# Performance work log

Measured on AMD Instinct MI355X. Metric: run time of the kernel, lower is better.

The kernel has to match this reference:

```python
import jax, jax.numpy as jnp
import numpy as np

D_MODEL = 1024
N_HEADS = 16
DFF = 4096
B, S = 2, 2048
EPS = 1e-6


def _dense_params(key, d_in, d_out):
    kw, kb = jax.random.split(key)
    w = jax.random.normal(kw, (d_in, d_out), jnp.float32) * 0.02
    b = jax.random.normal(kb, (d_out,), jnp.float32) * 0.02
    return w, b


def setup_inputs() -> dict:
    key = jax.random.key(0)
    ks = jax.random.split(key, 20)
    inp = {
        "x": jax.random.normal(ks[0], (B, S, D_MODEL), jnp.float32),
        "enc_output": jax.random.normal(ks[1], (B, S, D_MODEL), jnp.float32),
        # causal look-ahead mask: 1 where attention is NOT allowed
        "look_ahead_mask": jnp.triu(jnp.ones((S, S), jnp.float32), k=1)[None, None],
        "padding_mask": (jax.random.uniform(ks[2], (B, 1, 1, S)) < 0.1).astype(jnp.float32),
    }
    names = ["mha1_wq", "mha1_wk", "mha1_wv", "mha1_wo",
             "mha2_wq", "mha2_wk", "mha2_wv", "mha2_wo"]
    for i, n in enumerate(names):
        w, b = _dense_params(ks[3 + i], D_MODEL, D_MODEL)
        inp[n] = w
        inp[n.replace("w", "b")] = b
    inp["ffn_w1"], inp["ffn_b1"] = _dense_params(ks[11], D_MODEL, DFF)
    inp["ffn_w2"], inp["ffn_b2"] = _dense_params(ks[12], DFF, D_MODEL)
    for i, n in enumerate(["ln1", "ln2", "ln3"]):
        inp[n + "_g"] = jnp.ones((D_MODEL,), jnp.float32)
        inp[n + "_b"] = jnp.zeros((D_MODEL,), jnp.float32)
    return inp


def _layernorm(x, g, b):
    mu = jnp.mean(x, axis=-1, keepdims=True)
    var = jnp.mean(jnp.square(x - mu), axis=-1, keepdims=True)
    return (x - mu) * jax.lax.rsqrt(var + EPS) * g + b


def _mha(v, k, q, mask, wq, bq, wk, bk, wv, bv, wo, bo):
    Bq, Sq, D = q.shape
    depth = D // N_HEADS

    def split(t):  # [B,S,D] -> [B,H,S,depth]
        return t.reshape(t.shape[0], -1, N_HEADS, depth).transpose(0, 2, 1, 3)

    qh = split(q @ wq + bq)
    kh = split(k @ wk + bk)
    vh = split(v @ wv + bv)
    logits = jnp.einsum("bhqd,bhkd->bhqk", qh, kh) / jnp.sqrt(jnp.float32(depth))
    if mask is not None:
        logits = logits + mask * (-1e9)
    attn = jax.nn.softmax(logits, axis=-1)
    out = jnp.einsum("bhqk,bhkd->bhqd", attn, vh)
    out = out.transpose(0, 2, 1, 3).reshape(Bq, Sq, D)
    return out @ wo + bo


def reference(x, enc_output, look_ahead_mask, padding_mask,
              mha1_wq, mha1_bq, mha1_wk, mha1_bk, mha1_wv, mha1_bv, mha1_wo, mha1_bo,
              mha2_wq, mha2_bq, mha2_wk, mha2_bk, mha2_wv, mha2_bv, mha2_wo, mha2_bo,
              ffn_w1, ffn_b1, ffn_w2, ffn_b2,
              ln1_g, ln1_b, ln2_g, ln2_b, ln3_g, ln3_b):
    # self-attention (training=False -> dropout is identity)
    attn1 = _mha(x, x, x, look_ahead_mask,
                 mha1_wq, mha1_bq, mha1_wk, mha1_bk, mha1_wv, mha1_bv, mha1_wo, mha1_bo)
    out1 = _layernorm(x + attn1, ln1_g, ln1_b)
    # cross-attention: q from decoder, k/v from encoder output
    attn2 = _mha(enc_output, enc_output, out1, padding_mask,
                 mha2_wq, mha2_bq, mha2_wk, mha2_bk, mha2_wv, mha2_bv, mha2_wo, mha2_bo)
    out2 = _layernorm(out1 + attn2, ln2_g, ln2_b)
    ffn = jax.nn.relu(out2 @ ffn_w1 + ffn_b1) @ ffn_w2 + ffn_b2
    return _layernorm(out2 + ffn, ln3_g, ln3_b)
```

## Files before the change

### kernel.cpp

```cpp
#include <hip/hip_runtime.h>
#include <hip/hip_bf16.h>
#include <stdint.h>

#define DM   1024
#define NH   16
#define SS   2048
#define BB   2
#define MT   4096

typedef __attribute__((ext_vector_type(8))) short short8;
typedef __attribute__((ext_vector_type(4))) float f32x4;

typedef __attribute__((address_space(1))) const unsigned int as1_uint;
typedef __attribute__((address_space(3))) unsigned int as3_uint;

__device__ __forceinline__ void async16(const void* g, void* l) {
  __builtin_amdgcn_global_load_lds((as1_uint*)g, (as3_uint*)l, 16, 0, 0);
}

__device__ __forceinline__ unsigned short f2bf(float f) {
  union { float f; unsigned u; } c; c.f = f;
  unsigned r = c.u + 0x7fffu + ((c.u >> 16) & 1u);
  return (unsigned short)(r >> 16);
}

__device__ __forceinline__ unsigned cvt_pk_bf16(float lo, float hi) {
  unsigned r;
  asm("v_cvt_pk_bf16_f32 %0, %1, %2" : "=v"(r) : "v"(lo), "v"(hi));
  return r;
}

__global__ __launch_bounds__(256) void k_f32_to_bf16(
    const float* __restrict__ in, unsigned short* __restrict__ out, int n) {
  int i = (blockIdx.x * 256 + threadIdx.x) * 4;
  if (i >= n) return;
  float4 v = *(const float4*)(in + i);
  uint2 u;
  u.x = (unsigned)f2bf(v.x) | ((unsigned)f2bf(v.y) << 16);
  u.y = (unsigned)f2bf(v.z) | ((unsigned)f2bf(v.w) << 16);
  *(uint2*)(out + i) = u;
}

__global__ __launch_bounds__(256) void k_transpose_bf16(
    const float* __restrict__ in, unsigned short* __restrict__ out, int R, int C) {
  __shared__ float t[32][33];
  int c0 = blockIdx.x * 32, r0 = blockIdx.y * 32;
  int tx = threadIdx.x, ty = threadIdx.y;
#pragma unroll
  for (int i = 0; i < 4; i++)
    t[ty + i * 8][tx] = in[(size_t)(r0 + ty + i * 8) * C + c0 + tx];
  __syncthreads();
#pragma unroll
  for (int i = 0; i < 4; i++)
    out[(size_t)(c0 + ty + i * 8) * R + r0 + tx] = f2bf(t[tx][ty + i * 8]);
}

template<int BM, int OUT_MODE, bool RELU, bool RESID, bool SPLITK>
__global__ __launch_bounds__(256) void k_gemm(
    const unsigned short* __restrict__ A,
    const unsigned short* __restrict__ Bt,
    const float* __restrict__ bias,
    const float* __restrict__ resid,
    void* __restrict__ outp, void* __restrict__ outp2,
    int M, int N, int K, int KS) {
  __shared__ unsigned short Alds[2][BM * 32];
  __shared__ unsigned short Blds[2][128 * 32];
  int tid = threadIdx.x;
  int w = tid >> 6, lane = tid & 63;
  int l15 = lane & 15, l4 = lane >> 4;
  int brow = blockIdx.y * BM, bcol = blockIdx.x * 128;

  constexpr int MR = 4;
  constexpr int NR = (BM == 128) ? 4 : 2;
  int wr = (BM == 128) ? (w >> 1) : 0;
  int wc = (BM == 128) ? (w & 1) : w;
  int rbase = wr * 64;
  int cbase = wc * (NR * 16);

  f32x4 acc[MR][NR];
#pragma unroll
  for (int i = 0; i < MR; i++)
#pragma unroll
    for (int j = 0; j < NR; j++) acc[i][j] = (f32x4){0.f, 0.f, 0.f, 0.f};

#define STAGEG(bufi, kk) do {                                                  \
    _Pragma("unroll")                                                          \
    for (int c = 0; c < BM / 64; c++) {                                        \
      int elem = (c * 256 + tid) * 8;                                          \
      int row = elem >> 5, col = elem & 31;                                    \
      async16(A + (size_t)(brow + row) * K + (kk) + col, &Alds[bufi][elem]);   \
    }                                                                          \
    _Pragma("unroll")                                                          \
    for (int c = 0; c < 2; c++) {                                              \
      int elem = (c * 256 + tid) * 8;                                          \
      int row = elem >> 5, col = elem & 31;                                    \
      async16(Bt + (size_t)(bcol + row) * K + (kk) + col, &Blds[bufi][elem]);  \
    } } while (0)

  int kbeg = SPLITK ? blockIdx.z * KS : 0;
  int kend = kbeg + KS;
  STAGEG(0, kbeg);
  __syncthreads();
  int cur = 0;
  for (int k0 = kbeg; k0 < kend; k0 += 32) {
    if (k0 + 32 < kend) STAGEG(cur ^ 1, k0 + 32);
    short8 af[MR], bfr[NR];
#pragma unroll
    for (int i = 0; i < MR; i++)
      af[i] = *(const short8*)&Alds[cur][(rbase + i * 16 + l15) * 32 + l4 * 8];
#pragma unroll
    for (int j = 0; j < NR; j++)
      bfr[j] = *(const short8*)&Blds[cur][(cbase + j * 16 + l15) * 32 + l4 * 8];
#pragma unroll
    for (int i = 0; i < MR; i++)
#pragma unroll
      for (int j = 0; j < NR; j++)
        acc[i][j] = __builtin_amdgcn_mfma_f32_16x16x32_bf16(af[i], bfr[j], acc[i][j], 0, 0, 0);
    __syncthreads();
    cur ^= 1;
  }
#undef STAGEG

  void* op = (SPLITK && blockIdx.z) ? outp2 : outp;
#pragma unroll
  for (int i = 0; i < MR; i++)
#pragma unroll
    for (int j = 0; j < NR; j++) {
      int row = brow + rbase + i * 16 + l4 * 4;
      int col = bcol + cbase + j * 16 + l15;
      float bs = (SPLITK || !bias) ? 0.f : bias[col];
#pragma unroll
      for (int r = 0; r < 4; r++) {
        float v = acc[i][j][r] + bs;
        if (RESID) v += resid[(size_t)(row + r) * N + col];
        if (RELU) v = fmaxf(v, 0.f);
        if (OUT_MODE == 0) ((float*)op)[(size_t)(row + r) * N + col] = v;
        else               ((unsigned short*)op)[(size_t)(row + r) * N + col] = f2bf(v);
      }
    }
}

template<int NMAT>
__global__ __launch_bounds__(256) void k_gemm_qkv(
    const unsigned short* __restrict__ A,
    const unsigned short* __restrict__ Bt,
    const float* __restrict__ b0, const float* __restrict__ b1, const float* __restrict__ b2,
    unsigned short* __restrict__ o0, unsigned short* __restrict__ o1, unsigned short* __restrict__ o2,
    int vmat, int M, int K) {
  __shared__ unsigned short Alds[2][128 * 32];
  __shared__ unsigned short Blds[2][128 * 32];
  int tid = threadIdx.x;
  int w = tid >> 6, lane = tid & 63;
  int wr = w >> 1, wc = w & 1;
  int l15 = lane & 15, l4 = lane >> 4;
  int brow = blockIdx.y * 128, bcol = blockIdx.x * 128;

  f32x4 acc[4][4];
#pragma unroll
  for (int i = 0; i < 4; i++)
#pragma unroll
    for (int j = 0; j < 4; j++) acc[i][j] = (f32x4){0.f, 0.f, 0.f, 0.f};

#define STAGEQ(bufi, kk) do {                                                  \
    _Pragma("unroll")                                                          \
    for (int c = 0; c < 2; c++) {                                              \
      int elem = (c * 256 + tid) * 8;                                          \
      int row = elem >> 5, col = elem & 31;                                    \
      async16(A + (size_t)(brow + row) * K + (kk) + col, &Alds[bufi][elem]);   \
      async16(Bt + (size_t)(bcol + row) * K + (kk) + col, &Blds[bufi][elem]);  \
    } } while (0)

  STAGEQ(0, 0);
  __syncthreads();
  int cur = 0;
  for (int k0 = 0; k0 < K; k0 += 32) {
    if (k0 + 32 < K) STAGEQ(cur ^ 1, k0 + 32);
    short8 af[4], bfr[4];
#pragma unroll
    for (int i = 0; i < 4; i++) {
      af[i]  = *(const short8*)&Alds[cur][(wr * 64 + i * 16 + l15) * 32 + l4 * 8];
      bfr[i] = *(const short8*)&Blds[cur][(wc * 64 + i * 16 + l15) * 32 + l4 * 8];
    }
#pragma unroll
    for (int i = 0; i < 4; i++)
#pragma unroll
      for (int j = 0; j < 4; j++)
        acc[i][j] = __builtin_amdgcn_mfma_f32_16x16x32_bf16(af[i], bfr[j], acc[i][j], 0, 0, 0);
    __syncthreads();
    cur ^= 1;
  }
#undef STAGEQ

  int mat = bcol >> 10;
  const float* bias = (mat == 0) ? b0 : (mat == 1) ? b1 : b2;
  unsigned short* op = (mat == 0) ? o0 : (mat == 1) ? o1 : o2;
  int colSlab = bcol & 1023;
  bool tr = (mat == vmat);
#pragma unroll
  for (int i = 0; i < 4; i++)
#pragma unroll
    for (int j = 0; j < 4; j++) {
      int row = brow + wr * 64 + i * 16 + l4 * 4;
      int colL = colSlab + wc * 64 + j * 16 + l15;
      float bs = bias[colL];
#pragma unroll
      for (int r = 0; r < 4; r++) {
        float v = acc[i][j][r] + bs;
        if (tr) op[(size_t)colL * M + row + r] = f2bf(v);
        else    op[(size_t)(row + r) * 1024 + colL] = f2bf(v);
      }
    }
}

template<bool CAUSAL>
__global__ __launch_bounds__(256) void k_attn(
    const unsigned short* __restrict__ Q,
    const unsigned short* __restrict__ Kb,
    const unsigned short* __restrict__ Vt,
    const float* __restrict__ pm,
    unsigned short* __restrict__ out) {
  __shared__ unsigned short Klds[2][64 * 64];
  __shared__ unsigned short Vlds[2][64 * 64];
  __shared__ unsigned short Pw[4][2][16 * 72];
  int tid = threadIdx.x, w = tid >> 6, lane = tid & 63;
  int l15 = lane & 15, l4 = lane >> 4;
  int qt = CAUSAL ? ((int)gridDim.x - 1 - (int)blockIdx.x) : blockIdx.x;
  int h = blockIdx.y, b = blockIdx.z;
  int qbase = qt * 128 + w * 32;
  const float SC = 0.125f * 1.44269504089f;

  short8 qf[2][2];
#pragma unroll
  for (int f = 0; f < 2; f++) {
    size_t qrow = (size_t)b * SS + qbase + f * 16 + l15;
#pragma unroll
    for (int ks = 0; ks < 2; ks++)
      qf[f][ks] = *(const short8*)(Q + qrow * DM + h * 64 + ks * 32 + l4 * 8);
  }

  float mrow[2] = {-1e30f, -1e30f}, lrow[2] = {0.f, 0.f};
  f32x4 accO[2][4];
#pragma unroll
  for (int f = 0; f < 2; f++)
#pragma unroll
    for (int d = 0; d < 4; d++) accO[f][d] = (f32x4){0.f, 0.f, 0.f, 0.f};

#define STAGE(bufi, kt_) do {                                                  \
    _Pragma("unroll")                                                          \
    for (int c = 0; c < 2; c++) {                                              \
      int e0 = w * 1024 + c * 512;                                             \
      int elem = e0 + lane * 8;                                                \
      int row_ = elem >> 6;                                                    \
      int col_ = (elem & 63) ^ ((row_ & 7) << 3);                              \
      async16(Kb + (size_t)(b * SS + (kt_) * 64 + row_) * DM + h * 64 + col_,  \
              &Klds[bufi][elem]);                                              \
      async16(Vt + (size_t)(h * 64 + row_) * MT + b * SS + (kt_) * 64 + col_,  \
              &Vlds[bufi][elem]);                                              \
    } } while (0)

  int ktend = CAUSAL ? (2 * qt + 1) : (SS / 64 - 1);
  STAGE(0, 0);
  __syncthreads();
  int cur = 0;

  for (int kt = 0; kt <= ktend; kt++) {
    if (kt < ktend) STAGE(cur ^ 1, kt + 1);

    bool active = !CAUSAL || (kt * 64 <= qbase + 31);
    if (active) {
      f32x4 sa[2][4];
#pragma unroll
      for (int f = 0; f < 2; f++)
#pragma unroll
        for (int nt = 0; nt < 4; nt++) sa[f][nt] = (f32x4){0.f, 0.f, 0.f, 0.f};
      __builtin_amdgcn_s_setprio(1);
#pragma unroll
      for (int ks = 0; ks < 2; ks++)
#pragma unroll
        for (int nt = 0; nt < 4; nt++) {
          int kr = nt * 16 + l15;
          short8 kf = *(const short8*)&Klds[cur][kr * 64 + ((ks * 32 + l4 * 8) ^ ((kr & 7) << 3))];
#pragma unroll
          for (int f = 0; f < 2; f++)
            sa[f][nt] = __builtin_amdgcn_mfma_f32_16x16x32_bf16(kf, qf[f][ks], sa[f][nt], 0, 0, 0);
        }
      __builtin_amdgcn_s_setprio(0);

      float pmb[16];
      if (!CAUSAL) {
#pragma unroll
        for (int nt = 0; nt < 4; nt++) {
          float4 pmv = *(const float4*)(pm + b * SS + kt * 64 + nt * 16 + l4 * 4);
#pragma unroll
          for (int r = 0; r < 4; r++) pmb[nt * 4 + r] = ((const float*)&pmv)[r] * -1e30f;
        }
      }
      bool diag = CAUSAL && (kt * 64 + 63 > qbase);

#pragma unroll
      for (int f = 0; f < 2; f++) {
        float sv[16], tmax = -3e38f;
        if (CAUSAL && !diag) {
#pragma unroll
          for (int i = 0; i < 16; i++) {
            float s = sa[f][i >> 2][i & 3] * SC;
            sv[i] = s; tmax = fmaxf(tmax, s);
          }
        } else if (CAUSAL) {
#pragma unroll
          for (int nt = 0; nt < 4; nt++)
#pragma unroll
            for (int r = 0; r < 4; r++) {
              float s = sa[f][nt][r] * SC;
              int kg = kt * 64 + nt * 16 + l4 * 4 + r;
              int qg = qbase + f * 16 + l15;
              if (kg > qg) s = -1e30f;
              sv[nt * 4 + r] = s; tmax = fmaxf(tmax, s);
            }
        } else {
#pragma unroll
          for (int i = 0; i < 16; i++) {
            float s = fmaf(sa[f][i >> 2][i & 3], SC, pmb[i]);
            sv[i] = s; tmax = fmaxf(tmax, s);
          }
        }
        tmax = fmaxf(tmax, __shfl_xor(tmax, 16));
        tmax = fmaxf(tmax, __shfl_xor(tmax, 32));

        if (!__all(tmax - mrow[f] <= 8.f)) {
          float mnew = fmaxf(mrow[f], tmax);
          float corr = exp2f(mrow[f] - mnew);
          mrow[f] = mnew;
          lrow[f] *= corr;
#pragma unroll
          for (int r = 0; r < 4; r++) {
            float cq = __shfl(corr, l4 * 4 + r);
#pragma unroll
            for (int dt = 0; dt < 4; dt++) accO[f][dt][r] *= cq;
          }
        }

        float p[16], psum = 0.f;
#pragma unroll
        for (int i = 0; i < 16; i++) { p[i] = exp2f(sv[i] - mrow[f]); psum += p[i]; }
        psum += __shfl_xor(psum, 16);
        psum += __shfl_xor(psum, 32);
        lrow[f] += psum;

#pragma unroll
        for (int nt = 0; nt < 4; nt++) {
          uint2 u;
          u.x = cvt_pk_bf16(p[nt * 4 + 0], p[nt * 4 + 1]);
          u.y = cvt_pk_bf16(p[nt * 4 + 2], p[nt * 4 + 3]);
          *(uint2*)&Pw[w][f][l15 * 72 + nt * 16 + l4 * 4] = u;
        }
      }

      __builtin_amdgcn_s_setprio(1);
#pragma unroll
      for (int ks = 0; ks < 2; ks++) {
        short8 pf0 = *(const short8*)&Pw[w][0][l15 * 72 + ks * 32 + l4 * 8];
        short8 pf1 = *(const short8*)&Pw[w][1][l15 * 72 + ks * 32 + l4 * 8];
#pragma unroll
        for (int dt = 0; dt < 4; dt++) {
          int vr = dt * 16 + l15;
          short8 vf = *(const short8*)&Vlds[cur][vr * 64 + ((ks * 32 + l4 * 8) ^ ((vr & 7) << 3))];
          accO[0][dt] = __builtin_amdgcn_mfma_f32_16x16x32_bf16(pf0, vf, accO[0][dt], 0, 0, 0);
          accO[1][dt] = __builtin_amdgcn_mfma_f32_16x16x32_bf16(pf1, vf, accO[1][dt], 0, 0, 0);
        }
      }
      __builtin_amdgcn_s_setprio(0);
    }
    __syncthreads();
    cur ^= 1;
  }
#undef STAGE

#pragma unroll
  for (int f = 0; f < 2; f++)
#pragma unroll
    for (int r = 0; r < 4; r++) {
      float lq = __shfl(lrow[f], l4 * 4 + r);
      float inv = 1.f / lq;
      size_t row = (size_t)b * SS + qbase + f * 16 + l4 * 4 + r;
#pragma unroll
      for (int dt = 0; dt < 4; dt++)
        out[row * DM + h * 64 + dt * 16 + l15] = f2bf(accO[f][dt][r] * inv);
    }
}

__global__ __launch_bounds__(256) void k_ln(
    const float* __restrict__ in, const float* __restrict__ in2,
    const float* __restrict__ resid, const float* __restrict__ bias,
    const float* __restrict__ g, const float* __restrict__ bb,
    float* __restrict__ outf, unsigned short* __restrict__ outb) {
  int row = blockIdx.x, tid = threadIdx.x;
  int w = tid >> 6;
  __shared__ float red[4];
  float4 v = *(const float4*)(in + (size_t)row * 1024 + tid * 4);
  if (in2) {
    float4 v2 = *(const float4*)(in2 + (size_t)row * 1024 + tid * 4);
    v.x += v2.x; v.y += v2.y; v.z += v2.z; v.w += v2.w;
  }
  if (resid) {
    float4 v2 = *(const float4*)(resid + (size_t)row * 1024 + tid * 4);
    v.x += v2.x; v.y += v2.y; v.z += v2.z; v.w += v2.w;
  }
  if (bias) {
    float4 v2 = *(const float4*)(bias + tid * 4);
    v.x += v2.x; v.y += v2.y; v.z += v2.z; v.w += v2.w;
  }
  float s = v.x + v.y + v.z + v.w;
#pragma unroll
  for (int d = 1; d < 64; d <<= 1) s += __shfl_xor(s, d);
  if ((tid & 63) == 0) red[w] = s;
  __syncthreads();
  float mu = (red[0] + red[1] + red[2] + red[3]) * (1.f / 1024.f);
  float d0 = v.x - mu, d1 = v.y - mu, d2 = v.z - mu, d3 = v.w - mu;
  float q = d0 * d0 + d1 * d1 + d2 * d2 + d3 * d3;
#pragma unroll
  for (int d = 1; d < 64; d <<= 1) q += __shfl_xor(q, d);
  __syncthreads();
  if ((tid & 63) == 0) red[w] = q;
  __syncthreads();
  float var = (red[0] + red[1] + red[2] + red[3]) * (1.f / 1024.f);
  float rs = rsqrtf(var + 1e-6f);
  float4 gg = *(const float4*)(g + tid * 4);
  float4 bv = *(const float4*)(bb + tid * 4);
  float y0 = d0 * rs * gg.x + bv.x;
  float y1 = d1 * rs * gg.y + bv.y;
  float y2 = d2 * rs * gg.z + bv.z;
  float y3 = d3 * rs * gg.w + bv.w;
  if (outf) {
    float4 o; o.x = y0; o.y = y1; o.z = y2; o.w = y3;
    *(float4*)(outf + (size_t)row * 1024 + tid * 4) = o;
  }
  if (outb) {
    uint2 u;
    u.x = (unsigned)f2bf(y0) | ((unsigned)f2bf(y1) << 16);
    u.y = (unsigned)f2bf(y2) | ((unsigned)f2bf(y3) << 16);
    *(uint2*)(outb + (size_t)row * 1024 + tid * 4) = u;
  }
}

extern "C" void kernel_launch(void* const* d_in, const int* in_sizes, int n_in,
                              void* d_out, int out_size, void* d_ws, size_t ws_size,
                              hipStream_t stream) {
  const float* x    = (const float*)d_in[0];
  const float* enc  = (const float*)d_in[1];
  const float* pm   = (const float*)d_in[3];
  const float* wq1  = (const float*)d_in[4];   const float* bq1 = (const float*)d_in[5];
  const float* wk1  = (const float*)d_in[6];   const float* bk1 = (const float*)d_in[7];
  const float* wv1  = (const float*)d_in[8];   const float* bv1 = (const float*)d_in[9];
  const float* wo1  = (const float*)d_in[10];  const float* bo1 = (const float*)d_in[11];
  const float* wq2  = (const float*)d_in[12];  const float* bq2 = (const float*)d_in[13];
  const float* wk2  = (const float*)d_in[14];  const float* bk2 = (const float*)d_in[15];
  const float* wv2  = (const float*)d_in[16];  const float* bv2 = (const float*)d_in[17];
  const float* wo2  = (const float*)d_in[18];  const float* bo2 = (const float*)d_in[19];
  const float* fw1  = (const float*)d_in[20];  const float* fb1 = (const float*)d_in[21];
  const float* fw2  = (const float*)d_in[22];  const float* fb2 = (const float*)d_in[23];
  const float* ln1g = (const float*)d_in[24];  const float* ln1b = (const float*)d_in[25];
  const float* ln2g = (const float*)d_in[26];  const float* ln2b = (const float*)d_in[27];
  const float* ln3g = (const float*)d_in[28];  const float* ln3b = (const float*)d_in[29];

  char* ws = (char*)d_ws;
  unsigned short* XB = (unsigned short*)(ws + 0);
  unsigned short* EB = (unsigned short*)(ws + 8388608);
  unsigned short* Qb = (unsigned short*)(ws + 16777216);
  unsigned short* Kb = (unsigned short*)(ws + 25165824);
  unsigned short* Vt = (unsigned short*)(ws + 33554432);
  unsigned short* AT = (unsigned short*)(ws + 41943040);
  float*          T  = (float*)(ws + 50331648);
  float*          R  = (float*)(ws + 67108864);
  unsigned short* RB = (unsigned short*)(ws + 83886080);
  unsigned short* WT0 = (unsigned short*)(ws + 92274688);
  unsigned short* W1T = (unsigned short*)(ws + 92274688 + 16777216);
  unsigned short* W2T = (unsigned short*)(ws + 92274688 + 25165824);
  unsigned short* H   = (unsigned short*)(ws + 0);
  float*          T1  = (float*)(ws + 33554432);

  k_f32_to_bf16<<<4096, 256, 0, stream>>>(x, XB, MT * DM);
  k_f32_to_bf16<<<4096, 256, 0, stream>>>(enc, EB, MT * DM);
  dim3 tb(32, 8);
  const float* wlist[8] = {wq1, wk1, wv1, wo1, wq2, wk2, wv2, wo2};
  for (int i = 0; i < 8; i++)
    k_transpose_bf16<<<dim3(32, 32), tb, 0, stream>>>(wlist[i], WT0 + (size_t)i * 1048576, 1024, 1024);
  k_transpose_bf16<<<dim3(128, 32), tb, 0, stream>>>(fw1, W1T, 1024, 4096);
  k_transpose_bf16<<<dim3(32, 128), tb, 0, stream>>>(fw2, W2T, 4096, 1024);

  dim3 g64(8, 64), ga(16, 16, 2);

  k_gemm_qkv<3><<<dim3(24, 32), 256, 0, stream>>>(XB, WT0, bq1, bk1, bv1,
                                                  Qb, Kb, Vt, 2, MT, DM);
  k_attn<true><<<ga, 256, 0, stream>>>(Qb, Kb, Vt, nullptr, AT);
  k_gemm<64, 0, false, true, false><<<g64, 256, 0, stream>>>(
      AT, WT0 + 3 * 1048576, bo1, x, T, nullptr, MT, DM, DM, DM);
  k_ln<<<4096, 256, 0, stream>>>(T, nullptr, nullptr, nullptr, ln1g, ln1b, R, RB);

  k_gemm<64, 1, false, false, false><<<g64, 256, 0, stream>>>(
      RB, WT0 + 4 * 1048576, bq2, nullptr, Qb, nullptr, MT, DM, DM, DM);
  k_gemm_qkv<2><<<dim3(16, 32), 256, 0, stream>>>(EB, WT0 + 5 * 1048576, bk2, bv2, nullptr,
                                                  Kb, Vt, nullptr, 1, MT, DM);
  k_attn<false><<<ga, 256, 0, stream>>>(Qb, Kb, Vt, pm, AT);
  k_gemm<64, 0, false, true, false><<<g64, 256, 0, stream>>>(
      AT, WT0 + 7 * 1048576, bo2, R, T, nullptr, MT, DM, DM, DM);
  k_ln<<<4096, 256, 0, stream>>>(T, nullptr, nullptr, nullptr, ln2g, ln2b, R, RB);

  k_gemm<128, 1, true, false, false><<<dim3(32, 32), 256, 0, stream>>>(
      RB, W1T, fb1, nullptr, H, nullptr, MT, 4096, DM, DM);
  k_gemm<128, 0, false, false, true><<<dim3(8, 32, 2), 256, 0, stream>>>(
      H, W2T, nullptr, nullptr, T, T1, MT, DM, 4096, 2048);
  k_ln<<<4096, 256, 0, stream>>>(T, T1, R, fb2, ln3g, ln3b, (float*)d_out, nullptr);
}
```

Baseline: 507.0 us.

## Triple-buffer GEMM and attention loads, batch QKV via grid z, split-K out-projections

Replaces double buffering with a three-stage LDS ring in the GEMM, QKV GEMM and attention kernels. Each loop waits on vmcnt and issues a raw s_barrier instead of a full __syncthreads, so loads stay in flight two iterations ahead. The QKV kernel now picks its matrix from blockIdx.z, which lets the cross-attention Q, K and V projections run in one launch. The output projections become split-K GEMMs whose bias and residual are folded into the layernorm, and FFN2 uses the 64-row tile. The cost is more LDS per block, which may lower occupancy, and the hand-placed waitcnt depends on exact load counts being right.

```diff
diff --git a/kernel.cpp b/kernel.cpp
--- a/kernel.cpp
+++ b/kernel.cpp
@@ -17,6 +17,9 @@
 __device__ __forceinline__ void async16(const void* g, void* l) {
   __builtin_amdgcn_global_load_lds((as1_uint*)g, (as3_uint*)l, 16, 0, 0);
 }
+
+#define WAITV(n) asm volatile("s_waitcnt vmcnt(" #n ")" ::: "memory")
+#define BARRIER_SB() do { __builtin_amdgcn_s_barrier(); __builtin_amdgcn_sched_barrier(0); } while (0)
 
 __device__ __forceinline__ unsigned short f2bf(float f) {
   union { float f; unsigned u; } c; c.f = f;
@@ -63,8 +66,8 @@
     const float* __restrict__ resid,
     void* __restrict__ outp, void* __restrict__ outp2,
     int M, int N, int K, int KS) {
-  __shared__ unsigned short Alds[2][BM * 32];
-  __shared__ unsigned short Blds[2][128 * 32];
+  __shared__ unsigned short Alds[3][BM * 32];
+  __shared__ unsigned short Blds[3][128 * 32];
   int tid = threadIdx.x;
   int w = tid >> 6, lane = tid & 63;
   int l15 = lane & 15, l4 = lane >> 4;
@@ -98,26 +101,37 @@
     } } while (0)
 
   int kbeg = SPLITK ? blockIdx.z * KS : 0;
-  int kend = kbeg + KS;
+  int nk = KS / 32;
   STAGEG(0, kbeg);
-  __syncthreads();
-  int cur = 0;
-  for (int k0 = kbeg; k0 < kend; k0 += 32) {
-    if (k0 + 32 < kend) STAGEG(cur ^ 1, k0 + 32);
+  if (nk > 1) {
+    STAGEG(1, kbeg + 32);
+    if (BM == 128) WAITV(4); else WAITV(3);
+  } else {
+    WAITV(0);
+  }
+  BARRIER_SB();
+
+  for (int t = 0; t < nk; t++) {
+    int buf = t % 3;
+    if (t + 2 < nk) STAGEG((t + 2) % 3, kbeg + (t + 2) * 32);
     short8 af[MR], bfr[NR];
 #pragma unroll
     for (int i = 0; i < MR; i++)
-      af[i] = *(const short8*)&Alds[cur][(rbase + i * 16 + l15) * 32 + l4 * 8];
+      af[i] = *(const short8*)&Alds[buf][(rbase + i * 16 + l15) * 32 + l4 * 8];
 #pragma unroll
     for (int j = 0; j < NR; j++)
-      bfr[j] = *(const short8*)&Blds[cur][(cbase + j * 16 + l15) * 32 + l4 * 8];
+      bfr[j] = *(const short8*)&Blds[buf][(cbase + j * 16 + l15) * 32 + l4 * 8];
 #pragma unroll
     for (int i = 0; i < MR; i++)
 #pragma unroll
       for (int j = 0; j < NR; j++)
         acc[i][j] = __builtin_amdgcn_mfma_f32_16x16x32_bf16(af[i], bfr[j], acc[i][j], 0, 0, 0);
-    __syncthreads();
-    cur ^= 1;
+    if (t + 2 < nk) {
+      if (BM == 128) WAITV(4); else WAITV(3);
+    } else if (t + 1 < nk) {
+      WAITV(0);
+    }
+    if (t + 1 < nk) BARRIER_SB();
   }
 #undef STAGEG
 
@@ -140,19 +154,22 @@
     }
 }
 
-template<int NMAT>
 __global__ __launch_bounds__(256) void k_gemm_qkv(
-    const unsigned short* __restrict__ A,
+    const unsigned short* __restrict__ a0, const unsigned short* __restrict__ a1,
+    const unsigned short* __restrict__ a2,
     const unsigned short* __restrict__ Bt,
     const float* __restrict__ b0, const float* __restrict__ b1, const float* __restrict__ b2,
     unsigned short* __restrict__ o0, unsigned short* __restrict__ o1, unsigned short* __restrict__ o2,
     int vmat, int M, int K) {
-  __shared__ unsigned short Alds[2][128 * 32];
-  __shared__ unsigned short Blds[2][128 * 32];
+  __shared__ unsigned short Alds[3][128 * 32];
+  __shared__ unsigned short Blds[3][128 * 32];
   int tid = threadIdx.x;
   int w = tid >> 6, lane = tid & 63;
   int wr = w >> 1, wc = w & 1;
   int l15 = lane & 15, l4 = lane >> 4;
+  int z = blockIdx.z;
+  const unsigned short* A  = (z == 0) ? a0 : (z == 1) ? a1 : a2;
+  const unsigned short* Bz = Bt + (size_t)z * 1048576;
   int brow = blockIdx.y * 128, bcol = blockIdx.x * 128;
 
   f32x4 acc[4][4];
@@ -167,41 +184,44 @@
       int elem = (c * 256 + tid) * 8;                                          \
       int row = elem >> 5, col = elem & 31;                                    \
       async16(A + (size_t)(brow + row) * K + (kk) + col, &Alds[bufi][elem]);   \
-      async16(Bt + (size_t)(bcol + row) * K + (kk) + col, &Blds[bufi][elem]);  \
+      async16(Bz + (size_t)(bcol + row) * K + (kk) + col, &Blds[bufi][elem]);  \
     } } while (0)
 
+  int nk = K / 32;
   STAGEQ(0, 0);
-  __syncthreads();
-  int cur = 0;
-  for (int k0 = 0; k0 < K; k0 += 32) {
-    if (k0 + 32 < K) STAGEQ(cur ^ 1, k0 + 32);
+  STAGEQ(1, 32);
+  WAITV(4);
+  BARRIER_SB();
+
+  for (int t = 0; t < nk; t++) {
+    int buf = t % 3;
+    if (t + 2 < nk) STAGEQ((t + 2) % 3, (t + 2) * 32);
     short8 af[4], bfr[4];
 #pragma unroll
     for (int i = 0; i < 4; i++) {
-      af[i]  = *(const short8*)&Alds[cur][(wr * 64 + i * 16 + l15) * 32 + l4 * 8];
-      bfr[i] = *(const short8*)&Blds[cur][(wc * 64 + i * 16 + l15) * 32 + l4 * 8];
+      af[i]  = *(const short8*)&Alds[buf][(wr * 64 + i * 16 + l15) * 32 + l4 * 8];
+      bfr[i] = *(const short8*)&Blds[buf][(wc * 64 + i * 16 + l15) * 32 + l4 * 8];
     }
 #pragma unroll
     for (int i = 0; i < 4; i++)
 #pragma unroll
       for (int j = 0; j < 4; j++)
         acc[i][j] = __builtin_amdgcn_mfma_f32_16x16x32_bf16(af[i], bfr[j], acc[i][j], 0, 0, 0);
-    __syncthreads();
-    cur ^= 1;
+    if (t + 2 < nk) WAITV(4);
+    else if (t + 1 < nk) WAITV(0);
+    if (t + 1 < nk) BARRIER_SB();
   }
 #undef STAGEQ
 
-  int mat = bcol >> 10;
-  const float* bias = (mat == 0) ? b0 : (mat == 1) ? b1 : b2;
-  unsigned short* op = (mat == 0) ? o0 : (mat == 1) ? o1 : o2;
-  int colSlab = bcol & 1023;
-  bool tr = (mat == vmat);
+  const float* bias = (z == 0) ? b0 : (z == 1) ? b1 : b2;
+  unsigned short* op = (z == 0) ? o0 : (z == 1) ? o1 : o2;
+  bool tr = (z == vmat);
 #pragma unroll
   for (int i = 0; i < 4; i++)
 #pragma unroll
     for (int j = 0; j < 4; j++) {
       int row = brow + wr * 64 + i * 16 + l4 * 4;
-      int colL = colSlab + wc * 64 + j * 16 + l15;
+      int colL = bcol + wc * 64 + j * 16 + l15;
       float bs = bias[colL];
 #pragma unroll
       for (int r = 0; r < 4; r++) {
@@ -219,8 +239,8 @@
     const unsigned short* __restrict__ Vt,
     const float* __restrict__ pm,
     unsigned short* __restrict__ out) {
-  __shared__ unsigned short Klds[2][64 * 64];
-  __shared__ unsigned short Vlds[2][64 * 64];
+  __shared__ unsigned short Klds[3][64 * 64];
+  __shared__ unsigned short Vlds[3][64 * 64];
   __shared__ unsigned short Pw[4][2][16 * 72];
   int tid = threadIdx.x, w = tid >> 6, lane = tid & 63;
   int l15 = lane & 15, l4 = lane >> 4;
@@ -260,11 +280,12 @@
 
   int ktend = CAUSAL ? (2 * qt + 1) : (SS / 64 - 1);
   STAGE(0, 0);
-  __syncthreads();
-  int cur = 0;
+  if (ktend >= 1) { STAGE(1, 1); WAITV(4); } else { WAITV(0); }
+  BARRIER_SB();
 
   for (int kt = 0; kt <= ktend; kt++) {
-    if (kt < ktend) STAGE(cur ^ 1, kt + 1);
+    int buf = kt % 3;
+    if (kt + 2 <= ktend) STAGE((kt + 2) % 3, kt + 2);
 
     bool active = !CAUSAL || (kt * 64 <= qbase + 31);
     if (active) {
@@ -279,7 +300,7 @@
 #pragma unroll
         for (int nt = 0; nt < 4; nt++) {
           int kr = nt * 16 + l15;
-          short8 kf = *(const short8*)&Klds[cur][kr * 64 + ((ks * 32 + l4 * 8) ^ ((kr & 7) << 3))];
+          short8 kf = *(const short8*)&Klds[buf][kr * 64 + ((ks * 32 + l4 * 8) ^ ((kr & 7) << 3))];
 #pragma unroll
           for (int f = 0; f < 2; f++)
             sa[f][nt] = __builtin_amdgcn_mfma_f32_16x16x32_bf16(kf, qf[f][ks], sa[f][nt], 0, 0, 0);
@@ -364,15 +385,17 @@
 #pragma unroll
         for (int dt = 0; dt < 4; dt++) {
           int vr = dt * 16 + l15;
-          short8 vf = *(const short8*)&Vlds[cur][vr * 64 + ((ks * 32 + l4 * 8) ^ ((vr & 7) << 3))];
+          short8 vf = *(const short8*)&Vlds[buf][vr * 64 + ((ks * 32 + l4 * 8) ^ ((vr & 7) << 3))];
           accO[0][dt] = __builtin_amdgcn_mfma_f32_16x16x32_bf16(pf0, vf, accO[0][dt], 0, 0, 0);
           accO[1][dt] = __builtin_amdgcn_mfma_f32_16x16x32_bf16(pf1, vf, accO[1][dt], 0, 0, 0);
         }
       }
       __builtin_amdgcn_s_setprio(0);
     }
-    __syncthreads();
-    cur ^= 1;
+
+    if (kt + 2 <= ktend) WAITV(4);
+    else if (kt + 1 <= ktend) WAITV(0);
+    if (kt + 1 <= ktend) BARRIER_SB();
   }
 #undef STAGE
 
@@ -478,6 +501,7 @@
   unsigned short* W2T = (unsigned short*)(ws + 92274688 + 25165824);
   unsigned short* H   = (unsigned short*)(ws + 0);
   float*          T1  = (float*)(ws + 33554432);
+  float*          T1o = (float*)(ws + 16777216);
 
   k_f32_to_bf16<<<4096, 256, 0, stream>>>(x, XB, MT * DM);
   k_f32_to_bf16<<<4096, 256, 0, stream>>>(enc, EB, MT * DM);
@@ -488,27 +512,25 @@
   k_transpose_bf16<<<dim3(128, 32), tb, 0, stream>>>(fw1, W1T, 1024, 4096);
   k_transpose_bf16<<<dim3(32, 128), tb, 0, stream>>>(fw2, W2T, 4096, 1024);
 
-  dim3 g64(8, 64), ga(16, 16, 2);
-
-  k_gemm_qkv<3><<<dim3(24, 32), 256, 0, stream>>>(XB, WT0, bq1, bk1, bv1,
-                                                  Qb, Kb, Vt, 2, MT, DM);
+  dim3 ga(16, 16, 2);
+
+  k_gemm_qkv<<<dim3(8, 32, 3), 256, 0, stream>>>(XB, XB, XB, WT0, bq1, bk1, bv1,
+                                                 Qb, Kb, Vt, 2, MT, DM);
   k_attn<true><<<ga, 256, 0, stream>>>(Qb, Kb, Vt, nullptr, AT);
-  k_gemm<64, 0, false, true, false><<<g64, 256, 0, stream>>>(
-      AT, WT0 + 3 * 1048576, bo1, x, T, nullptr, MT, DM, DM, DM);
-  k_ln<<<4096, 256, 0, stream>>>(T, nullptr, nullptr, nullptr, ln1g, ln1b, R, RB);
-
-  k_gemm<64, 1, false, false, false><<<g64, 256, 0, stream>>>(
-      RB, WT0 + 4 * 1048576, bq2, nullptr, Qb, nullptr, MT, DM, DM, DM);
-  k_gemm_qkv<2><<<dim3(16, 32), 256, 0, stream>>>(EB, WT0 + 5 * 1048576, bk2, bv2, nullptr,
-                                                  Kb, Vt, nullptr, 1, MT, DM);
+  k_gemm<64, 0, false, false, true><<<dim3(8, 64, 2), 256, 0, stream>>>(
+      AT, WT0 + 3 * 1048576, nullptr, nullptr, T, T1o, MT, DM, DM, 512);
+  k_ln<<<4096, 256, 0, stream>>>(T, T1o, x, bo1, ln1g, ln1b, R, RB);
+
+  k_gemm_qkv<<<dim3(8, 32, 3), 256, 0, stream>>>(RB, EB, EB, WT0 + 4 * 1048576,
+                                                 bq2, bk2, bv2, Qb, Kb, Vt, 2, MT, DM);
   k_attn<false><<<ga, 256, 0, stream>>>(Qb, Kb, Vt, pm, AT);
-  k_gemm<64, 0, false, true, false><<<g64, 256, 0, stream>>>(
-      AT, WT0 + 7 * 1048576, bo2, R, T, nullptr, MT, DM, DM, DM);
-  k_ln<<<4096, 256, 0, stream>>>(T, nullptr, nullptr, nullptr, ln2g, ln2b, R, RB);
+  k_gemm<64, 0, false, false, true><<<dim3(8, 64, 2), 256, 0, stream>>>(
+      AT, WT0 + 7 * 1048576, nullptr, nullptr, T, T1o, MT, DM, DM, 512);
+  k_ln<<<4096, 256, 0, stream>>>(T, T1o, R, bo2, ln2g, ln2b, R, RB);
 
   k_gemm<128, 1, true, false, false><<<dim3(32, 32), 256, 0, stream>>>(
-      RB, W1T, fb1, nullptr, H, nullptr, MT, 4096, DM, DM);
-  k_gemm<128, 0, false, false, true><<<dim3(8, 32, 2), 256, 0, stream>>>(
+      RB, W1T, fb1, nullptr, H, nullptr, MT, 4096, DM, 1024);
+  k_gemm<64, 0, false, false, true><<<dim3(8, 64, 2), 256, 0, stream>>>(
       H, W2T, nullptr, nullptr, T, T1, MT, DM, 4096, 2048);
   k_ln<<<4096, 256, 0, stream>>>(T, T1, R, fb2, ln3g, ln3b, (float*)d_out, nullptr);
 }
```

New measurement: 507.4 us. About the same (+0.1%).
